# Optimization experiments

Hardware: AMD Instinct MI355X
Metric: run time of the kernel (lower is better)

Reference implementation:

```python
import jax, jax.numpy as jnp
import numpy as np

D_MODEL = 2048
D_STATE = 128
D_CONV = 4
NHEADS = 64
NGROUPS = 1
HEAD_DIM = 64
CHUNK = 128
EPS = 1e-5
D_INNER = NHEADS * HEAD_DIM                       # 4096
CONV_DIM = D_INNER + 2 * NGROUPS * D_STATE        # 4352
D_IN_PROJ = 2 * D_INNER + 2 * NGROUPS * D_STATE + NHEADS  # 8512


def setup_inputs() -> dict:
    key = jax.random.key(0)
    ks = jax.random.split(key, 9)
    B, S = 2, 4096
    return dict(
        hidden_states=jax.random.normal(ks[0], (B, S, D_MODEL), jnp.float32),
        W_in=jax.random.normal(ks[1], (D_MODEL, D_IN_PROJ), jnp.float32) * 0.02,
        conv_w=jax.random.normal(ks[2], (CONV_DIM, D_CONV), jnp.float32) * 0.2,
        conv_b=jax.random.normal(ks[3], (CONV_DIM,), jnp.float32) * 0.1,
        # A must be negative (stable SSM): A = -exp(u), u ~ U[0,2)
        A=-jnp.exp(jax.random.uniform(ks[4], (NHEADS,), jnp.float32, 0.0, 2.0)),
        D=jax.random.normal(ks[5], (NHEADS,), jnp.float32),
        dt_bias=jax.random.normal(ks[6], (NHEADS,), jnp.float32),
        norm_w=jnp.ones((D_INNER,), jnp.float32),
        W_out=jax.random.normal(ks[7], (D_INNER, D_MODEL), jnp.float32) * 0.02,
    )


def _silu(x):
    return x * jax.nn.sigmoid(x)


def _causal_conv1d(x, w, b):
    # depthwise causal conv with silu; x [B,S,C], w [C,K], b [C]
    K = w.shape[1]
    S = x.shape[1]
    xp = jnp.pad(x, ((0, 0), (K - 1, 0), (0, 0)))
    y = sum(xp[:, k:k + S, :] * w[None, None, :, k].swapaxes(-1, -1) for k in range(0))
    y = jnp.zeros_like(x)
    for k in range(K):
        y = y + xp[:, k:k + S, :] * w[:, k][None, None, :]
    return _silu(y + b)


def _ssd(x, dt, A, Bm, Cm, chunk):
    # Mamba2 chunked SSD scan.
    # x [b,s,h,p]; dt [b,s,h] (>0); A [h]; Bm,Cm [b,s,g,n]
    b, s, h, p = x.shape
    g, n = Bm.shape[2], Bm.shape[3]
    hh = h // g
    c = s // chunk
    x = x.reshape(b, c, chunk, g, hh, p)
    dt = dt.reshape(b, c, chunk, g, hh)
    Bm = Bm.reshape(b, c, chunk, g, n)
    Cm = Cm.reshape(b, c, chunk, g, n)
    dA = dt * A.reshape(g, hh)                 # [b,c,l,g,hh]
    dA_cs = jnp.cumsum(dA, axis=2)             # [b,c,l,g,hh]
    dtx = dt[..., None] * x                    # [b,c,l,g,hh,p]
    # intra-chunk (diagonal blocks): L[i,j] = exp(sum_{j<k<=i} dA)
    diff = dA_cs[:, :, :, None] - dA_cs[:, :, None, :]   # [b,c,i,j,g,hh]
    mask = jnp.tril(jnp.ones((chunk, chunk), bool))
    L = jnp.exp(jnp.where(mask[None, None, :, :, None, None], diff, -jnp.inf))
    Y = jnp.einsum('bcign,bcjgn,bcijgh,bcjghp->bcighp', Cm, Bm, L, dtx)
    # chunk-final states
    decay = jnp.exp(dA_cs[:, :, -1:] - dA_cs)            # [b,c,l,g,hh]
    states = jnp.einsum('bcjgn,bcjgh,bcjghp->bcghpn', Bm, decay, dtx)
    chunk_decay = jnp.exp(dA_cs[:, :, -1])               # [b,c,g,hh]
    def step(prev, inp):
        cd, st = inp
        return cd[..., None, None] * prev + st, prev
    init = jnp.zeros_like(states[:, 0])
    _, prevs = jax.lax.scan(step, init,
                            (jnp.moveaxis(chunk_decay, 1, 0), jnp.moveaxis(states, 1, 0)))
    prevs = jnp.moveaxis(prevs, 0, 1)                    # [b,c,g,hh,p,n] state entering each chunk
    Y = Y + jnp.einsum('bcign,bcghpn,bcigh->bcighp', Cm, prevs, jnp.exp(dA_cs))
    return Y.reshape(b, s, h, p)


def reference(hidden_states, W_in, conv_w, conv_b, A, D, dt_bias, norm_w, W_out):
    Bsz, S, _ = hidden_states.shape
    zxbcdt = hidden_states @ W_in                        # [B,S,d_in_proj]
    z = zxbcdt[..., :D_INNER]
    xbc = zxbcdt[..., D_INNER:D_INNER + CONV_DIM]
    dt = zxbcdt[..., D_INNER + CONV_DIM:]                # [B,S,nheads]
    xbc = _causal_conv1d(xbc, conv_w, conv_b)            # silu-activated causal conv
    x = xbc[..., :D_INNER].reshape(Bsz, S, NHEADS, HEAD_DIM)
    Bm = xbc[..., D_INNER:D_INNER + NGROUPS * D_STATE].reshape(Bsz, S, NGROUPS, D_STATE)
    Cm = xbc[..., D_INNER + NGROUPS * D_STATE:].reshape(Bsz, S, NGROUPS, D_STATE)
    dt = jax.nn.softplus(dt + dt_bias)                   # delta_softplus, dt_limit=(0,inf)
    y = _ssd(x, dt, A, Bm, Cm, CHUNK)
    y = y + D[None, None, :, None] * x                   # skip (D) term
    y = y.reshape(Bsz, S, D_INNER)
    # gated RMSNorm (norm_before_gate=False): normalize(y * silu(z)), grouped
    yg = y * _silu(z)
    gsz = D_INNER // NGROUPS
    ygr = yg.reshape(Bsz, S, NGROUPS, gsz)
    rms = jax.lax.rsqrt(jnp.mean(ygr * ygr, axis=-1, keepdims=True) + EPS)
    yn = (ygr * rms).reshape(Bsz, S, D_INNER) * norm_w
    return yn @ W_out
```

## Files before the change

### kernel.cpp

```cpp
#include <hip/hip_runtime.h>
#include <hip/hip_bf16.h>

typedef __bf16 bf16_t;
typedef bf16_t bf16x8 __attribute__((ext_vector_type(8)));
typedef float f32x4 __attribute__((ext_vector_type(4)));

#define TOK 8192
#define DMODEL 2048
#define DINNER 4096
#define XBCN 4352
#define DSTATE 128
#define NH 64
#define HD 64
#define NBC 64
#define WINT_ROWS 8448

__device__ __forceinline__ void gld16(const bf16_t* g, bf16_t* l) {
  __builtin_amdgcn_global_load_lds((const __attribute__((address_space(1))) void*)g,
                                   (__attribute__((address_space(3))) void*)l, 16, 0, 0);
}

__device__ __forceinline__ f32x4 mfma16(bf16x8 a, bf16x8 b, f32x4 c) {
  return __builtin_amdgcn_mfma_f32_16x16x32_bf16(a, b, c, 0, 0, 0);
}

__device__ __forceinline__ bf16x8 ldsr(unsigned addr) {
  f32x4 r;
  asm volatile("ds_read_b128 %0, %1" : "=v"(r) : "v"(addr));
  return __builtin_bit_cast(bf16x8, r);
}


__global__ __launch_bounds__(256)
void cast_split_kernel(const float* __restrict__ in, bf16_t* __restrict__ hi,
                       bf16_t* __restrict__ lo, size_t n) {
  size_t i = ((size_t)blockIdx.x * 256 + threadIdx.x) * 8;
  if (i + 8 > n) return;
  float4 a = *(const float4*)(in + i);
  float4 b = *(const float4*)(in + i + 4);
  float v[8] = {a.x,a.y,a.z,a.w,b.x,b.y,b.z,b.w};
  bf16x8 h, l;
#pragma unroll
  for (int j = 0; j < 8; ++j) {
    h[j] = (bf16_t)v[j];
    l[j] = (bf16_t)(v[j] - (float)h[j]);
  }
  *(bf16x8*)(hi + i) = h;
  *(bf16x8*)(lo + i) = l;
}

__global__ __launch_bounds__(256)
void transpose_cast_kernel(const float* __restrict__ in, bf16_t* __restrict__ out,
                           int R, int C, int outRows) {
  __shared__ float tile[32][33];
  const int c0 = blockIdx.x * 32;
  const int r0 = blockIdx.y * 32;
  const int tx = threadIdx.x & 31;
  const int ty = threadIdx.x >> 5;
#pragma unroll
  for (int k = 0; k < 4; ++k) {
    int r = r0 + ty + k*8;
    int c = c0 + tx;
    tile[ty + k*8][tx] = (c < C) ? in[(size_t)r * C + c] : 0.f;
  }
  __syncthreads();
#pragma unroll
  for (int k = 0; k < 4; ++k) {
    int oc = c0 + ty + k*8;
    int orr = r0 + tx;
    out[(size_t)oc * R + orr] = (bf16_t)tile[tx][ty + k*8];
  }
}

__global__ __launch_bounds__(256)
void wdt_split_kernel(const float* __restrict__ Win, bf16_t* __restrict__ Whi,
                      bf16_t* __restrict__ Wlo) {
  const int h = threadIdx.x & 63;
  const int k0 = blockIdx.x * 256 + (threadIdx.x >> 6) * 64;
#pragma unroll 4
  for (int i = 0; i < 64; ++i) {
    int k = k0 + i;
    float v = Win[(size_t)k * 8512 + 8448 + h];
    bf16_t hv = (bf16_t)v;
    Whi[(size_t)h * DMODEL + k] = hv;
    Wlo[(size_t)h * DMODEL + k] = (bf16_t)(v - (float)hv);
  }
}

template <typename OutT>
__global__ __launch_bounds__(512, 2)
void gemm256(const bf16_t* __restrict__ A, const bf16_t* __restrict__ B,
             OutT* __restrict__ C0, OutT* __restrict__ C1,
             long M, long N, long K, long splitN, int gridX) {
  __shared__ bf16_t sA[2][2][8192];
  __shared__ bf16_t sB[2][2][8192];
  const int tid = threadIdx.x;
  const int lane = tid & 63;
  const int wid = tid >> 6;
  const int wr = wid >> 2;
  const int wc = wid & 3;

  const int x = blockIdx.x & 7;
  const int q = blockIdx.x >> 3;
  const long bm = (long)(x * 4 + (q & 3)) * 256;
  const long bn = (long)(q >> 2) * 256;

  const int srow = (wid >> 1) * 16 + (lane & 15);
  const int skof = (wid & 1) * 32 + (lane >> 4) * 8;
  const bf16_t* Abase = A + (bm + srow) * K + skof;
  const bf16_t* Bbase = B + (bn + srow) * K + skof;

  auto stageA = [&](int buf, int h, long kt) {
    const bf16_t* s = Abase + (long)h * 128 * K + kt;
    gld16(s,          &sA[buf][h][wid * 512]);
    gld16(s + 64 * K, &sA[buf][h][4096 + wid * 512]);
  };
  auto stageB = [&](int buf, int h, long kt) {
    const bf16_t* s = Bbase + (long)h * 128 * K + kt;
    gld16(s,          &sB[buf][h][wid * 512]);
    gld16(s + 64 * K, &sB[buf][h][4096 + wid * 512]);
  };

  const unsigned sAb = (unsigned)(uintptr_t)(__attribute__((address_space(3))) void*)&sA[0][0][0]
                       + (unsigned)lane * 16 + (unsigned)wr * 8192;
  const unsigned sBb = (unsigned)(uintptr_t)(__attribute__((address_space(3))) void*)&sB[0][0][0]
                       + (unsigned)lane * 16 + (unsigned)wc * 4096;

  stageA(0, 0, 0); stageB(0, 0, 0); stageB(0, 1, 0); stageA(0, 1, 0);

  f32x4 acc[8][4] = {};
  bf16x8 a[4][2], b[2][2];
  int cur = 0;
  const int NT = (int)(K >> 6);

  for (int t = 0; t < NT; ++t) {
    const bool fin = (t == NT - 1);
    const long ktn = (long)(t + 1) * 64;
    const unsigned ab0 = sAb + (unsigned)cur * 32768;
    const unsigned bb0 = sBb + (unsigned)cur * 32768;

    asm volatile("s_waitcnt vmcnt(4)\n\ts_barrier" ::: "memory");
    if (!fin) stageA(cur ^ 1, 0, ktn);
#pragma unroll
    for (int mi = 0; mi < 4; ++mi) {
      a[mi][0] = ldsr(ab0 + (mi*2+0)*1024);
      a[mi][1] = ldsr(ab0 + (mi*2+1)*1024);
    }
#pragma unroll
    for (int ni = 0; ni < 2; ++ni) {
      b[ni][0] = ldsr(bb0 + (ni*2+0)*1024);
      b[ni][1] = ldsr(bb0 + (ni*2+1)*1024);
    }
    asm volatile("s_waitcnt lgkmcnt(0)" ::: "memory");
    __builtin_amdgcn_sched_barrier(0);
    __builtin_amdgcn_s_setprio(1);
#pragma unroll
    for (int mi = 0; mi < 4; ++mi)
#pragma unroll
      for (int ni = 0; ni < 2; ++ni) {
        acc[mi][ni] = mfma16(a[mi][0], b[ni][0], acc[mi][ni]);
        acc[mi][ni] = mfma16(a[mi][1], b[ni][1], acc[mi][ni]);
      }
    __builtin_amdgcn_s_setprio(0);
    __builtin_amdgcn_sched_barrier(0);

    if (!fin) asm volatile("s_waitcnt vmcnt(4)\n\ts_barrier" ::: "memory");
    else      asm volatile("s_waitcnt vmcnt(2)\n\ts_barrier" ::: "memory");
    if (!fin) stageB(cur ^ 1, 0, ktn);
#pragma unroll
    for (int ni = 0; ni < 2; ++ni) {
      b[ni][0] = ldsr(bb0 + 16384 + (ni*2+0)*1024);
      b[ni][1] = ldsr(bb0 + 16384 + (ni*2+1)*1024);
    }
    asm volatile("s_waitcnt lgkmcnt(0)" ::: "memory");
    __builtin_amdgcn_sched_barrier(0);
    __builtin_amdgcn_s_setprio(1);
#pragma unroll
    for (int mi = 0; mi < 4; ++mi)
#pragma unroll
      for (int ni = 0; ni < 2; ++ni) {
        acc[mi][2 + ni] = mfma16(a[mi][0], b[ni][0], acc[mi][2 + ni]);
        acc[mi][2 + ni] = mfma16(a[mi][1], b[ni][1], acc[mi][2 + ni]);
      }
    __builtin_amdgcn_s_setprio(0);
    __builtin_amdgcn_sched_barrier(0);

    if (!fin) asm volatile("s_waitcnt vmcnt(4)\n\ts_barrier" ::: "memory");
    else      asm volatile("s_waitcnt vmcnt(0)\n\ts_barrier" ::: "memory");
    if (!fin) stageB(cur ^ 1, 1, ktn);
#pragma unroll
    for (int mi = 0; mi < 4; ++mi) {
      a[mi][0] = ldsr(ab0 + 16384 + (mi*2+0)*1024);
      a[mi][1] = ldsr(ab0 + 16384 + (mi*2+1)*1024);
    }
    asm volatile("s_waitcnt lgkmcnt(0)" ::: "memory");
    __builtin_amdgcn_sched_barrier(0);
    __builtin_amdgcn_s_setprio(1);
#pragma unroll
    for (int mi = 0; mi < 4; ++mi)
#pragma unroll
      for (int ni = 0; ni < 2; ++ni) {
        acc[4 + mi][2 + ni] = mfma16(a[mi][0], b[ni][0], acc[4 + mi][2 + ni]);
        acc[4 + mi][2 + ni] = mfma16(a[mi][1], b[ni][1], acc[4 + mi][2 + ni]);
      }
    __builtin_amdgcn_s_setprio(0);
    __builtin_amdgcn_sched_barrier(0);

    asm volatile("s_barrier" ::: "memory");
    if (!fin) stageA(cur ^ 1, 1, ktn);
#pragma unroll
    for (int ni = 0; ni < 2; ++ni) {
      b[ni][0] = ldsr(bb0 + (ni*2+0)*1024);
      b[ni][1] = ldsr(bb0 + (ni*2+1)*1024);
    }
    asm volatile("s_waitcnt lgkmcnt(0)" ::: "memory");
    __builtin_amdgcn_sched_barrier(0);
    __builtin_amdgcn_s_setprio(1);
#pragma unroll
    for (int mi = 0; mi < 4; ++mi)
#pragma unroll
      for (int ni = 0; ni < 2; ++ni) {
        acc[4 + mi][ni] = mfma16(a[mi][0], b[ni][0], acc[4 + mi][ni]);
        acc[4 + mi][ni] = mfma16(a[mi][1], b[ni][1], acc[4 + mi][ni]);
      }
    __builtin_amdgcn_s_setprio(0);
    __builtin_amdgcn_sched_barrier(0);
    cur ^= 1;
  }

  const int cr = (lane >> 4) * 4;
  const int cc = lane & 15;
  OutT* Cb;
  long col0, ldc;
  if (bn < splitN) { Cb = C0; col0 = bn; ldc = splitN; }
  else             { Cb = C1; col0 = bn - splitN; ldc = N - splitN; }
#pragma unroll
  for (int mi = 0; mi < 8; ++mi) {
    long row = bm + (mi >> 2) * 128 + wr * 64 + (mi & 3) * 16 + cr;
#pragma unroll
    for (int ni = 0; ni < 4; ++ni) {
      long col = col0 + (ni >> 1) * 128 + wc * 32 + (ni & 1) * 16 + cc;
      OutT* p = Cb + row * ldc + col;
#pragma unroll
      for (int r = 0; r < 4; ++r) p[(long)r * ldc] = (OutT)acc[mi][ni][r];
    }
  }
}

__global__ __launch_bounds__(256)
void dt_mfma_kernel(const bf16_t* __restrict__ Ahi, const bf16_t* __restrict__ Alo,
                    const bf16_t* __restrict__ Whi, const bf16_t* __restrict__ Wlo,
                    float* __restrict__ dtraw) {
  __shared__ bf16_t sAh[4096], sAl[4096], sBh[2048], sBl[2048];
  const int tid = threadIdx.x;
  const int lane = tid & 63;
  const int w = tid >> 6;
  const long bm = (long)blockIdx.x * 128;
  const int rlo = lane & 15;
  const int kq = lane >> 4;

  const bf16_t* Ah0 = Ahi + (bm + 2*w*16 + rlo) * (long)DMODEL + kq*8;
  const bf16_t* Ah1 = Ah0 + 16*(long)DMODEL;
  const bf16_t* Al0 = Alo + (bm + 2*w*16 + rlo) * (long)DMODEL + kq*8;
  const bf16_t* Al1 = Al0 + 16*(long)DMODEL;
  const bf16_t* Bh0 = Whi + (w*16 + rlo) * (long)DMODEL + kq*8;
  const bf16_t* Bl0 = Wlo + (w*16 + rlo) * (long)DMODEL + kq*8;

  f32x4 acc[2][4] = {};

  for (int kt = 0; kt < DMODEL; kt += 32) {
    __syncthreads();
    gld16(Ah0 + kt, &sAh[(2*w)*512]);
    gld16(Ah1 + kt, &sAh[(2*w+1)*512]);
    gld16(Al0 + kt, &sAl[(2*w)*512]);
    gld16(Al1 + kt, &sAl[(2*w+1)*512]);
    gld16(Bh0 + kt, &sBh[w*512]);
    gld16(Bl0 + kt, &sBl[w*512]);
    __syncthreads();
    bf16x8 ah[2], al[2], bh[4], bl[4];
#pragma unroll
    for (int i = 0; i < 2; ++i) {
      ah[i] = *(const bf16x8*)&sAh[((2*w + i)*64 + lane)*8];
      al[i] = *(const bf16x8*)&sAl[((2*w + i)*64 + lane)*8];
    }
#pragma unroll
    for (int n = 0; n < 4; ++n) {
      bh[n] = *(const bf16x8*)&sBh[(n*64 + lane)*8];
      bl[n] = *(const bf16x8*)&sBl[(n*64 + lane)*8];
    }
#pragma unroll
    for (int mi = 0; mi < 2; ++mi)
#pragma unroll
      for (int n = 0; n < 4; ++n) {
        acc[mi][n] = mfma16(ah[mi], bh[n], acc[mi][n]);
        acc[mi][n] = mfma16(ah[mi], bl[n], acc[mi][n]);
        acc[mi][n] = mfma16(al[mi], bh[n], acc[mi][n]);
      }
  }

  const int cr = (lane >> 4) * 4;
  const int cc = lane & 15;
#pragma unroll
  for (int mi = 0; mi < 2; ++mi)
#pragma unroll
    for (int n = 0; n < 4; ++n)
#pragma unroll
      for (int r = 0; r < 4; ++r)
        dtraw[(bm + 2*w*16 + mi*16 + cr + r) * 64 + n*16 + cc] = acc[mi][n][r];
}

__global__ __launch_bounds__(256)
void conv_kernel(const bf16_t* __restrict__ xbc, const float* __restrict__ cw,
                 const float* __restrict__ cb, bf16_t* __restrict__ xo,
                 bf16_t* __restrict__ Bout, bf16_t* __restrict__ Cout) {
  const int c = blockIdx.x * 256 + threadIdx.x;
  const int t0 = blockIdx.y * 8;
  const int bstart = (t0 >> 12) << 12;
  const float w0 = cw[c*4+0], w1 = cw[c*4+1], w2 = cw[c*4+2], w3 = cw[c*4+3];
  const float bias = cb[c];
  float in[11];
#pragma unroll
  for (int k = 0; k < 11; ++k) {
    int t = t0 - 3 + k;
    in[k] = (t >= bstart) ? (float)xbc[(size_t)t * XBCN + c] : 0.f;
  }
#pragma unroll
  for (int i = 0; i < 8; ++i) {
    float v = bias + w0*in[i] + w1*in[i+1] + w2*in[i+2] + w3*in[i+3];
    float s = v / (1.f + __expf(-v));
    int t = t0 + i;
    bf16_t o = (bf16_t)s;
    if (c < DINNER)           xo[(size_t)t * DINNER + c] = o;
    else if (c < DINNER+128)  Bout[(size_t)t * DSTATE + (c - DINNER)] = o;
    else                      Cout[(size_t)t * DSTATE + (c - DINNER - 128)] = o;
  }
}

__global__ __launch_bounds__(256)
void dt_scan_kernel(const float* __restrict__ dtraw, const float* __restrict__ dt_bias,
                    const float* __restrict__ Avec, float* __restrict__ dt_s,
                    float* __restrict__ dAcs, float* __restrict__ cdec) {
  const int wid = blockIdx.x * 4 + (threadIdx.x >> 6);
  const int lane = threadIdx.x & 63;
  const int h = wid & 63;
  const int bc = wid >> 6;
  const long tok0 = (long)bc * 128;
  const float Ah = Avec[h];
  const float bias = dt_bias[h];
  float v0 = dtraw[(tok0 + lane)*64 + h] + bias;
  float v1 = dtraw[(tok0 + 64 + lane)*64 + h] + bias;
  float d0 = (v0 > 20.f) ? v0 : log1pf(expf(v0));
  float d1 = (v1 > 20.f) ? v1 : log1pf(expf(v1));
  float s0 = d0 * Ah;
  float s1 = d1 * Ah;
#pragma unroll
  for (int off = 1; off < 64; off <<= 1) {
    float t = __shfl_up(s0, off);
    if (lane >= off) s0 += t;
  }
  float tot0 = __shfl(s0, 63);
#pragma unroll
  for (int off = 1; off < 64; off <<= 1) {
    float t = __shfl_up(s1, off);
    if (lane >= off) s1 += t;
  }
  s1 += tot0;
  const size_t base = (size_t)wid * 128;
  dt_s[base + lane] = d0;
  dt_s[base + 64 + lane] = d1;
  dAcs[base + lane] = s0;
  dAcs[base + 64 + lane] = s1;
  if (lane == 63) cdec[wid] = __expf(s1);
}

__global__ __launch_bounds__(256)
void states_kernel(const bf16_t* __restrict__ x, const bf16_t* __restrict__ Bm,
                   const float* __restrict__ dt_s, const float* __restrict__ dAcs,
                   bf16_t* __restrict__ states) {
  __shared__ bf16_t sDtx[8192];
  __shared__ bf16_t sBd[16384];
  __shared__ float sDt[128];
  __shared__ float sDec[128];
  const int wid = blockIdx.x;
  const int h = wid & 63;
  const int bc = wid >> 6;
  const int tid = threadIdx.x;
  const int lane = tid & 63;
  const int w = tid >> 6;
  const long tok0 = (long)bc * 128;
  const size_t dbase = (size_t)wid * 128;

  if (tid < 128) {
    sDt[tid] = dt_s[dbase + tid];
  } else {
    int j = tid - 128;
    sDec[j] = __expf(dAcs[dbase + 127] - dAcs[dbase + j]);
  }
  __syncthreads();

  {
    const int jj0 = tid >> 3;
    const int pg = (tid & 7) * 8;
#pragma unroll
    for (int t = 0; t < 4; ++t) {
      int j = t*32 + jj0;
      bf16x8 xv = *(const bf16x8*)&x[(tok0 + j)*(long)DINNER + h*64 + pg];
      float dtj = sDt[j];
      int kq = (j >> 5) * 4;
      int qe = ((j >> 3) & 3) * 16;
      int e = j & 7;
#pragma unroll
      for (int i = 0; i < 8; ++i) {
        int p = pg + i;
        sDtx[((kq + (p>>4))*64 + qe + (p&15))*8 + e] = (bf16_t)((float)xv[i]*dtj);
      }
    }
    const int jj1 = tid >> 4;
    const int ng = (tid & 15) * 8;
#pragma unroll
    for (int t = 0; t < 8; ++t) {
      int j = t*16 + jj1;
      bf16x8 bv = *(const bf16x8*)&Bm[(tok0 + j)*(long)DSTATE + ng];
      float dec = sDec[j];
      int kq = (j >> 5) * 8;
      int qe = ((j >> 3) & 3) * 16;
      int e = j & 7;
#pragma unroll
      for (int i = 0; i < 8; ++i) {
        int n = ng + i;
        sBd[((kq + (n>>4))*64 + qe + (n&15))*8 + e] = (bf16_t)((float)bv[i]*dec);
      }
    }
  }
  __syncthreads();

  f32x4 acc[4][2] = {};
#pragma unroll
  for (int kt = 0; kt < 4; ++kt) {
    bf16x8 aF[4], bF[2];
#pragma unroll
    for (int mt = 0; mt < 4; ++mt) aF[mt] = *(const bf16x8*)&sDtx[((kt*4 + mt)*64 + lane)*8];
#pragma unroll
    for (int nt = 0; nt < 2; ++nt) bF[nt] = *(const bf16x8*)&sBd[((kt*8 + w*2 + nt)*64 + lane)*8];
#pragma unroll
    for (int mt = 0; mt < 4; ++mt)
#pragma unroll
      for (int nt = 0; nt < 2; ++nt)
        acc[mt][nt] = mfma16(aF[mt], bF[nt], acc[mt][nt]);
  }

  bf16_t* S = states + (size_t)wid * (HD * DSTATE);
  const int cr = (lane >> 4) * 4;
  const int cc = lane & 15;
#pragma unroll
  for (int mt = 0; mt < 4; ++mt)
#pragma unroll
    for (int nt = 0; nt < 2; ++nt) {
      int n = (w*2 + nt)*16 + cc;
#pragma unroll
      for (int r = 0; r < 4; ++r) {
        int p = mt*16 + cr + r;
        S[(size_t)p*DSTATE + n] = (bf16_t)acc[mt][nt][r];
      }
    }
}

__global__ __launch_bounds__(256)
void scan_kernel(bf16_t* __restrict__ sp, const float* __restrict__ cdec) {
  const size_t gid = (size_t)blockIdx.x * 256 + threadIdx.x;
  const int n = gid & 127;
  const int p = (gid >> 7) & 63;
  const int h = (gid >> 13) & 63;
  const int b = (int)(gid >> 19);
  float prev = 0.f;
  const size_t pn = (size_t)p * 128 + n;
  for (int c = 0; c < 32; ++c) {
    const int wid = (b*32 + c)*64 + h;
    const size_t idx = (size_t)wid * 8192 + pn;
    float s = (float)sp[idx];
    sp[idx] = (bf16_t)prev;
    prev = cdec[wid] * prev + s;
  }
}

__global__ __launch_bounds__(256)
void ssd_y_kernel(bf16_t* __restrict__ xy, const bf16_t* __restrict__ Bm,
                  const bf16_t* __restrict__ Cm, const bf16_t* __restrict__ prevs,
                  const float* __restrict__ dt_s, const float* __restrict__ dAcs,
                  const float* __restrict__ Dvec) {
  __shared__ bf16_t sG[16384];
  __shared__ bf16_t sDtx[8192];
  __shared__ float sDA[128];
  __shared__ float sEA[128];
  __shared__ float sDt[128];

  const int wid = blockIdx.x;
  const int h = wid & 63;
  const int bc = wid >> 6;
  const int tid = threadIdx.x;
  const int lane = tid & 63;
  const int w = tid >> 6;
  const long tok0 = (long)bc * 128;
  const size_t dbase = (size_t)wid * 128;

  if (tid < 128) {
    float v = dAcs[dbase + tid];
    sDA[tid] = v;
    sEA[tid] = __expf(v);
  } else {
    sDt[tid - 128] = dt_s[dbase + tid - 128];
  }
  __syncthreads();

  {
    const int jj0 = tid >> 3;
    const int pg = (tid & 7) * 8;
#pragma unroll
    for (int t = 0; t < 4; ++t) {
      int j = t*32 + jj0;
      bf16x8 xv = *(const bf16x8*)&xy[(tok0 + j)*(long)DINNER + h*64 + pg];
      float dtj = sDt[j];
      int kq = (j >> 5) * 4;
      int qe = ((j >> 3) & 3) * 16;
      int e = j & 7;
#pragma unroll
      for (int i = 0; i < 8; ++i) {
        int p = pg + i;
        sDtx[((kq + (p>>4))*64 + qe + (p&15))*8 + e] = (bf16_t)((float)xv[i]*dtj);
      }
    }
  }

  const int arow = (w*2)*16 + (lane & 15);
  const int koff = (lane >> 4) * 8;
  bf16x8 aCm[2][4];
#pragma unroll
  for (int mi = 0; mi < 2; ++mi)
#pragma unroll
    for (int kt = 0; kt < 4; ++kt)
      aCm[mi][kt] = *(const bf16x8*)&Cm[(tok0 + arow + mi*16)*(long)DSTATE + kt*32 + koff];

  const bf16_t* P = prevs + (size_t)wid * 8192;
  f32x4 accY[2][4] = {};
#pragma unroll
  for (int kt = 0; kt < 4; ++kt) {
    bf16x8 bP[4];
#pragma unroll
    for (int ni = 0; ni < 4; ++ni)
      bP[ni] = *(const bf16x8*)&P[(size_t)(ni*16 + (lane & 15))*DSTATE + kt*32 + koff];
#pragma unroll
    for (int mi = 0; mi < 2; ++mi)
#pragma unroll
      for (int ni = 0; ni < 4; ++ni)
        accY[mi][ni] = mfma16(aCm[mi][kt], bP[ni], accY[mi][ni]);
  }
  const int cr = (lane >> 4) * 4;
  const int cc = lane & 15;
#pragma unroll
  for (int mi = 0; mi < 2; ++mi)
#pragma unroll
    for (int r = 0; r < 4; ++r) {
      float e = sEA[(w*2 + mi)*16 + cr + r];
#pragma unroll
      for (int ni = 0; ni < 4; ++ni) accY[mi][ni][r] *= e;
    }

  f32x4 accS[2][8] = {};
#pragma unroll
  for (int kt = 0; kt < 4; ++kt) {
    bf16x8 bB[8];
#pragma unroll
    for (int nt = 0; nt < 8; ++nt)
      bB[nt] = *(const bf16x8*)&Bm[(tok0 + nt*16 + (lane & 15))*(long)DSTATE + kt*32 + koff];
#pragma unroll
    for (int mi = 0; mi < 2; ++mi)
#pragma unroll
      for (int nt = 0; nt < 8; ++nt)
        accS[mi][nt] = mfma16(aCm[mi][kt], bB[nt], accS[mi][nt]);
  }

#pragma unroll
  for (int mi = 0; mi < 2; ++mi)
#pragma unroll
    for (int nt = 0; nt < 8; ++nt)
#pragma unroll
      for (int r = 0; r < 4; ++r) {
        int i = (w*2 + mi)*16 + cr + r;
        int j = nt*16 + cc;
        float g = (i >= j) ? accS[mi][nt][r] * __expf(sDA[i] - sDA[j]) : 0.f;
        sG[(((j>>5)*8 + (i>>4))*64 + ((j>>3)&3)*16 + (i&15))*8 + (j&7)] = (bf16_t)g;
      }
  __syncthreads();

#pragma unroll
  for (int kt = 0; kt < 4; ++kt) {
    bf16x8 aG[2], bD[4];
#pragma unroll
    for (int mi = 0; mi < 2; ++mi) aG[mi] = *(const bf16x8*)&sG[((kt*8 + w*2 + mi)*64 + lane)*8];
#pragma unroll
    for (int ni = 0; ni < 4; ++ni) bD[ni] = *(const bf16x8*)&sDtx[((kt*4 + ni)*64 + lane)*8];
#pragma unroll
    for (int mi = 0; mi < 2; ++mi)
#pragma unroll
      for (int ni = 0; ni < 4; ++ni)
        accY[mi][ni] = mfma16(aG[mi], bD[ni], accY[mi][ni]);
  }

  const float Dh = Dvec[h];
#pragma unroll
  for (int mi = 0; mi < 2; ++mi)
#pragma unroll
    for (int ni = 0; ni < 4; ++ni)
#pragma unroll
      for (int r = 0; r < 4; ++r) {
        long tokr = tok0 + (w*2 + mi)*16 + cr + r;
        int p = ni*16 + cc;
        long idx = tokr * DINNER + h*64 + p;
        float xv = (float)xy[idx];
        xy[idx] = (bf16_t)(accY[mi][ni][r] + Dh * xv);
      }
}

__global__ __launch_bounds__(256)
void gate_kernel(const bf16_t* __restrict__ y, const bf16_t* __restrict__ z,
                 const float* __restrict__ norm_w, bf16_t* __restrict__ yn) {
  const int tok = blockIdx.x;
  const int tid = threadIdx.x;
  const int lane = tid & 63;
  const int w = tid >> 6;
  const bf16_t* yrow = y + (size_t)tok * DINNER;
  const bf16_t* zrow = z + (size_t)tok * DINNER;
  float local[16];
  float ss = 0.f;
#pragma unroll
  for (int v = 0; v < 2; ++v) {
    int col = tid*16 + v*8;
    bf16x8 yv = *(const bf16x8*)&yrow[col];
    bf16x8 zv = *(const bf16x8*)&zrow[col];
#pragma unroll
    for (int i = 0; i < 8; ++i) {
      float zf = (float)zv[i];
      float g = zf / (1.f + __expf(-zf));
      float t = (float)yv[i] * g;
      local[v*8 + i] = t;
      ss += t*t;
    }
  }
#pragma unroll
  for (int off = 32; off > 0; off >>= 1) ss += __shfl_xor(ss, off);
  __shared__ float red[4];
  if (lane == 0) red[w] = ss;
  __syncthreads();
  float rms = rsqrtf((red[0]+red[1]+red[2]+red[3]) * (1.f/DINNER) + 1e-5f);
  bf16_t* orow = yn + (size_t)tok * DINNER;
#pragma unroll
  for (int v = 0; v < 2; ++v) {
    int col = tid*16 + v*8;
    bf16x8 o;
#pragma unroll
    for (int i = 0; i < 8; ++i) o[i] = (bf16_t)(local[v*8+i] * rms * norm_w[col+i]);
    *(bf16x8*)&orow[col] = o;
  }
}

extern "C" void kernel_launch(void* const* d_in, const int* in_sizes, int n_in,
                              void* d_out, int out_size, void* d_ws, size_t ws_size,
                              hipStream_t stream) {
  const float* hidden  = (const float*)d_in[0];
  const float* W_in    = (const float*)d_in[1];
  const float* conv_w  = (const float*)d_in[2];
  const float* conv_b  = (const float*)d_in[3];
  const float* Avec    = (const float*)d_in[4];
  const float* Dvec    = (const float*)d_in[5];
  const float* dt_bias = (const float*)d_in[6];
  const float* norm_w  = (const float*)d_in[7];
  const float* W_out   = (const float*)d_in[8];

  char* ws = (char*)d_ws;
  size_t off = 0;
  auto take = [&](size_t bytes) -> char* {
    char* p = ws + off;
    off += (bytes + 255) & ~(size_t)255;
    return p;
  };
  bf16_t* R1    = (bf16_t*)take((size_t)NBC * NH * HD * DSTATE * 2);
  bf16_t* WinT  = (bf16_t*)take((size_t)WINT_ROWS * DMODEL * 2);
  bf16_t* xbc   = (bf16_t*)take((size_t)TOK * XBCN * 2);
  bf16_t* xconv = (bf16_t*)take((size_t)TOK * DINNER * 2);
  bf16_t* Bmat  = (bf16_t*)take((size_t)TOK * DSTATE * 2);
  bf16_t* Cmat  = (bf16_t*)take((size_t)TOK * DSTATE * 2);
  float*  dtraw = (float*)take((size_t)TOK * NH * 4);
  float*  dt_s  = (float*)take((size_t)TOK * NH * 4);
  float*  dAcs  = (float*)take((size_t)TOK * NH * 4);
  float*  cdec  = (float*)take((size_t)NBC * NH * 4);
  bf16_t* Wdth  = (bf16_t*)take((size_t)NH * DMODEL * 2);
  bf16_t* Wdtl  = (bf16_t*)take((size_t)NH * DMODEL * 2);
  if (off > ws_size) return;

  bf16_t* Xb      = R1;
  bf16_t* Xlo     = xbc;
  bf16_t* statesB = R1;
  bf16_t* ynbuf   = R1;
  bf16_t* WoutT   = WinT;
  bf16_t* zbuf    = (bf16_t*)d_out;
  float*  out     = (float*)d_out;

  cast_split_kernel<<<(TOK*DMODEL)/2048, 256, 0, stream>>>(hidden, Xb, Xlo, (size_t)TOK*DMODEL);
  wdt_split_kernel<<<DMODEL/256, 256, 0, stream>>>(W_in, Wdth, Wdtl);
  dt_mfma_kernel<<<TOK/128, 256, 0, stream>>>(Xb, Xlo, Wdth, Wdtl, dtraw);
  transpose_cast_kernel<<<dim3(WINT_ROWS/32, DMODEL/32), 256, 0, stream>>>(W_in, WinT, DMODEL, 8512, WINT_ROWS);
  gemm256<bf16_t><<<(TOK/256)*(WINT_ROWS/256), 512, 0, stream>>>(
      Xb, WinT, zbuf, xbc, TOK, WINT_ROWS, DMODEL, DINNER, WINT_ROWS/256);
  transpose_cast_kernel<<<dim3(DMODEL/32, DINNER/32), 256, 0, stream>>>(W_out, WoutT, DINNER, DMODEL, DMODEL);
  conv_kernel<<<dim3(XBCN/256, TOK/8), 256, 0, stream>>>(xbc, conv_w, conv_b, xconv, Bmat, Cmat);
  dt_scan_kernel<<<(NBC*NH)/4, 256, 0, stream>>>(dtraw, dt_bias, Avec, dt_s, dAcs, cdec);
  states_kernel<<<NBC*NH, 256, 0, stream>>>(xconv, Bmat, dt_s, dAcs, statesB);
  scan_kernel<<<(NBC*NH*HD*DSTATE)/(32*256), 256, 0, stream>>>(statesB, cdec);
  ssd_y_kernel<<<NBC*NH, 256, 0, stream>>>(xconv, Bmat, Cmat, statesB, dt_s, dAcs, Dvec);
  gate_kernel<<<TOK, 256, 0, stream>>>(xconv, zbuf, norm_w, ynbuf);
  gemm256<float><<<(TOK/256)*(DMODEL/256), 512, 0, stream>>>(
      ynbuf, WoutT, out, out, TOK, DMODEL, DINNER, DMODEL, DMODEL/256);
}
```

Baseline: 990.0 us.

## Restructure GEMM k-loop to one barrier per tile with separate fragment registers

The GEMM main loop goes from four barrier-separated quarter phases to a single barrier per k-tile. A and B fragments for both halves are held in separate registers, so each LDS fragment is read once instead of re-reading B. All next-tile global-to-LDS loads are issued early, overlapping the remaining LDS reads and MFMAs. This cuts barrier and wait overhead but raises register pressure, and the full vmcnt(0) wait at the top of each iteration may expose more global load latency.

```diff
diff --git a/kernel.cpp b/kernel.cpp
--- a/kernel.cpp
+++ b/kernel.cpp
@@ -129,99 +129,86 @@
   stageA(0, 0, 0); stageB(0, 0, 0); stageB(0, 1, 0); stageA(0, 1, 0);
 
   f32x4 acc[8][4] = {};
-  bf16x8 a[4][2], b[2][2];
+  bf16x8 a0[4][2], a1[4][2], b0[2][2], b1[2][2];
   int cur = 0;
   const int NT = (int)(K >> 6);
 
   for (int t = 0; t < NT; ++t) {
     const bool fin = (t == NT - 1);
     const long ktn = (long)(t + 1) * 64;
-    const unsigned ab0 = sAb + (unsigned)cur * 32768;
-    const unsigned bb0 = sBb + (unsigned)cur * 32768;
-
-    asm volatile("s_waitcnt vmcnt(4)\n\ts_barrier" ::: "memory");
-    if (!fin) stageA(cur ^ 1, 0, ktn);
+    const unsigned ab = sAb + (unsigned)cur * 32768;
+    const unsigned bb = sBb + (unsigned)cur * 32768;
+
+    asm volatile("s_waitcnt vmcnt(0)\n\ts_barrier" ::: "memory");
+
 #pragma unroll
     for (int mi = 0; mi < 4; ++mi) {
-      a[mi][0] = ldsr(ab0 + (mi*2+0)*1024);
-      a[mi][1] = ldsr(ab0 + (mi*2+1)*1024);
+      a0[mi][0] = ldsr(ab + (mi*2+0)*1024);
+      a0[mi][1] = ldsr(ab + (mi*2+1)*1024);
     }
 #pragma unroll
     for (int ni = 0; ni < 2; ++ni) {
-      b[ni][0] = ldsr(bb0 + (ni*2+0)*1024);
-      b[ni][1] = ldsr(bb0 + (ni*2+1)*1024);
-    }
+      b0[ni][0] = ldsr(bb + (ni*2+0)*1024);
+      b0[ni][1] = ldsr(bb + (ni*2+1)*1024);
+    }
+    if (!fin) { stageA(cur ^ 1, 0, ktn); stageB(cur ^ 1, 0, ktn); }
     asm volatile("s_waitcnt lgkmcnt(0)" ::: "memory");
     __builtin_amdgcn_sched_barrier(0);
+
+#pragma unroll
+    for (int ni = 0; ni < 2; ++ni) {
+      b1[ni][0] = ldsr(bb + 16384 + (ni*2+0)*1024);
+      b1[ni][1] = ldsr(bb + 16384 + (ni*2+1)*1024);
+    }
+    if (!fin) stageB(cur ^ 1, 1, ktn);
+    __builtin_amdgcn_sched_barrier(0);
     __builtin_amdgcn_s_setprio(1);
 #pragma unroll
     for (int mi = 0; mi < 4; ++mi)
 #pragma unroll
       for (int ni = 0; ni < 2; ++ni) {
-        acc[mi][ni] = mfma16(a[mi][0], b[ni][0], acc[mi][ni]);
-        acc[mi][ni] = mfma16(a[mi][1], b[ni][1], acc[mi][ni]);
+        acc[mi][ni] = mfma16(a0[mi][0], b0[ni][0], acc[mi][ni]);
+        acc[mi][ni] = mfma16(a0[mi][1], b0[ni][1], acc[mi][ni]);
       }
     __builtin_amdgcn_s_setprio(0);
     __builtin_amdgcn_sched_barrier(0);
-
-    if (!fin) asm volatile("s_waitcnt vmcnt(4)\n\ts_barrier" ::: "memory");
-    else      asm volatile("s_waitcnt vmcnt(2)\n\ts_barrier" ::: "memory");
-    if (!fin) stageB(cur ^ 1, 0, ktn);
-#pragma unroll
-    for (int ni = 0; ni < 2; ++ni) {
-      b[ni][0] = ldsr(bb0 + 16384 + (ni*2+0)*1024);
-      b[ni][1] = ldsr(bb0 + 16384 + (ni*2+1)*1024);
-    }
     asm volatile("s_waitcnt lgkmcnt(0)" ::: "memory");
     __builtin_amdgcn_sched_barrier(0);
+
+#pragma unroll
+    for (int mi = 0; mi < 4; ++mi) {
+      a1[mi][0] = ldsr(ab + 16384 + (mi*2+0)*1024);
+      a1[mi][1] = ldsr(ab + 16384 + (mi*2+1)*1024);
+    }
+    if (!fin) stageA(cur ^ 1, 1, ktn);
+    __builtin_amdgcn_sched_barrier(0);
     __builtin_amdgcn_s_setprio(1);
 #pragma unroll
     for (int mi = 0; mi < 4; ++mi)
 #pragma unroll
       for (int ni = 0; ni < 2; ++ni) {
-        acc[mi][2 + ni] = mfma16(a[mi][0], b[ni][0], acc[mi][2 + ni]);
-        acc[mi][2 + ni] = mfma16(a[mi][1], b[ni][1], acc[mi][2 + ni]);
+        acc[mi][2 + ni] = mfma16(a0[mi][0], b1[ni][0], acc[mi][2 + ni]);
+        acc[mi][2 + ni] = mfma16(a0[mi][1], b1[ni][1], acc[mi][2 + ni]);
       }
     __builtin_amdgcn_s_setprio(0);
     __builtin_amdgcn_sched_barrier(0);
-
-    if (!fin) asm volatile("s_waitcnt vmcnt(4)\n\ts_barrier" ::: "memory");
-    else      asm volatile("s_waitcnt vmcnt(0)\n\ts_barrier" ::: "memory");
-    if (!fin) stageB(cur ^ 1, 1, ktn);
-#pragma unroll
-    for (int mi = 0; mi < 4; ++mi) {
-      a[mi][0] = ldsr(ab0 + 16384 + (mi*2+0)*1024);
-      a[mi][1] = ldsr(ab0 + 16384 + (mi*2+1)*1024);
-    }
     asm volatile("s_waitcnt lgkmcnt(0)" ::: "memory");
     __builtin_amdgcn_sched_barrier(0);
+
     __builtin_amdgcn_s_setprio(1);
 #pragma unroll
     for (int mi = 0; mi < 4; ++mi)
 #pragma unroll
       for (int ni = 0; ni < 2; ++ni) {
-        acc[4 + mi][2 + ni] = mfma16(a[mi][0], b[ni][0], acc[4 + mi][2 + ni]);
-        acc[4 + mi][2 + ni] = mfma16(a[mi][1], b[ni][1], acc[4 + mi][2 + ni]);
-      }
-    __builtin_amdgcn_s_setprio(0);
-    __builtin_amdgcn_sched_barrier(0);
-
-    asm volatile("s_barrier" ::: "memory");
-    if (!fin) stageA(cur ^ 1, 1, ktn);
-#pragma unroll
-    for (int ni = 0; ni < 2; ++ni) {
-      b[ni][0] = ldsr(bb0 + (ni*2+0)*1024);
-      b[ni][1] = ldsr(bb0 + (ni*2+1)*1024);
-    }
-    asm volatile("s_waitcnt lgkmcnt(0)" ::: "memory");
-    __builtin_amdgcn_sched_barrier(0);
-    __builtin_amdgcn_s_setprio(1);
+        acc[4 + mi][2 + ni] = mfma16(a1[mi][0], b1[ni][0], acc[4 + mi][2 + ni]);
+        acc[4 + mi][2 + ni] = mfma16(a1[mi][1], b1[ni][1], acc[4 + mi][2 + ni]);
+      }
 #pragma unroll
     for (int mi = 0; mi < 4; ++mi)
 #pragma unroll
       for (int ni = 0; ni < 2; ++ni) {
-        acc[4 + mi][ni] = mfma16(a[mi][0], b[ni][0], acc[4 + mi][ni]);
-        acc[4 + mi][ni] = mfma16(a[mi][1], b[ni][1], acc[4 + mi][ni]);
+        acc[4 + mi][ni] = mfma16(a1[mi][0], b0[ni][0], acc[4 + mi][ni]);
+        acc[4 + mi][ni] = mfma16(a1[mi][1], b0[ni][1], acc[4 + mi][ni]);
       }
     __builtin_amdgcn_s_setprio(0);
     __builtin_amdgcn_sched_barrier(0);
```

Measured after the change: 1.053 ms. 1.06x slower.
